# Performance work log

Measured on AMD Instinct MI355X. Metric: run time of the kernel, lower is better.

Reference implementation:

```python
import jax, jax.numpy as jnp
import numpy as np

K = 1024          # num_embeddings
D = 64            # embedding_dim
COMMIT = 0.25
DIVERSITY = 0.1


def setup_inputs() -> dict:
    key = jax.random.key(0)
    k1, k2 = jax.random.split(key)
    inputs = jax.random.normal(k1, (64, D, 32, 32), dtype=jnp.float32)
    emb = jax.random.uniform(k2, (K, D), dtype=jnp.float32,
                             minval=-1.0 / K, maxval=1.0 / K)
    return {"inputs": inputs, "emb": emb}


def reference(inputs, emb):
    # NCHW -> NHWC, flatten to [N, D]
    x = jnp.transpose(inputs, (0, 2, 3, 1))          # [B,H,W,D]
    flat = x.reshape(-1, D)                           # [N,D]

    dist = (jnp.sum(flat * flat, axis=1, keepdims=True)
            + jnp.sum(emb * emb, axis=1)
            - 2.0 * flat @ emb.T)
    idx = jnp.argmin(dist, axis=1)                    # [N]
    encodings = jax.nn.one_hot(idx, K, dtype=flat.dtype)  # [N,K]

    # codebook lookup (equivalent to encodings @ emb)
    quantized = jnp.take(emb, idx, axis=0).reshape(x.shape)  # [B,H,W,D]

    sg = jax.lax.stop_gradient
    e_latent_loss = jnp.mean((sg(quantized) - x) ** 2)
    q_latent_loss = jnp.mean((quantized - sg(x)) ** 2)

    avg_probs = jnp.mean(encodings, axis=0)           # [K]
    perplexity = jnp.exp(-jnp.sum(avg_probs * jnp.log(avg_probs + 1e-10)))
    diversity_loss = DIVERSITY * (K - perplexity) / K

    loss = q_latent_loss + COMMIT * e_latent_loss + diversity_loss

    # straight-through estimator
    quantized_st = x + sg(quantized - x)
    quant_out = jnp.transpose(quantized_st, (0, 3, 1, 2))  # NHWC -> NCHW

    return loss, quant_out, perplexity, encodings, idx[:, None]
```

## Files before the change

### kernel.cpp

```cpp
#include <hip/hip_runtime.h>
#include <math.h>

typedef _Float16 half8 __attribute__((ext_vector_type(8)));
typedef float floatx4 __attribute__((ext_vector_type(4)));

namespace {
constexpr int Kc = 1024;
constexpr int Dd = 64;
constexpr float MARGIN = 4e-4f;

__device__ inline float np_sumsq64_s(const float* __restrict__ a, int st) {
#pragma clang fp contract(off)
    float r[8];
    #pragma unroll
    for (int j = 0; j < 8; ++j) r[j] = a[j * st] * a[j * st];
    #pragma unroll
    for (int i = 8; i < 64; i += 8) {
        #pragma unroll
        for (int j = 0; j < 8; ++j) {
            float s = a[(i + j) * st] * a[(i + j) * st];
            r[j] = r[j] + s;
        }
    }
    return ((r[0] + r[1]) + (r[2] + r[3])) + ((r[4] + r[5]) + (r[6] + r[7]));
}

__device__ inline float np_dist(const float* __restrict__ x, int xs,
                                const float* __restrict__ emb, int k,
                                float xx, float eek) {
    const float* e = emb + (size_t)k * Dd;
    float g = 0.f;
    #pragma unroll
    for (int d = 0; d < Dd; ++d) g = fmaf(x[d * xs], e[d], g);
    float A = xx + eek;
    return fmaf(-2.f, g, A);
}

__global__ void k_prep(const float* __restrict__ emb, float* __restrict__ ee,
                       _Float16* __restrict__ emb16) {
    int k = blockIdx.x * blockDim.x + threadIdx.x;
    const float* e = emb + (size_t)k * Dd;
    ee[k] = np_sumsq64_s(e, 1);
    #pragma unroll
    for (int d = 0; d < Dd; ++d) emb16[k * Dd + d] = (_Float16)e[d];
}

__global__ __launch_bounds__(256, 4) void k_main(
    const float* __restrict__ inputs, const float* __restrict__ emb,
    const float* __restrict__ ee_g, const _Float16* __restrict__ emb16,
    float* __restrict__ quant, float* __restrict__ enc, float* __restrict__ idx_out,
    unsigned int* __restrict__ hist, float* __restrict__ partials)
{
    __shared__ float eeS[Kc];
    __shared__ float cD[64][16][2];
    __shared__ int   cI[64][16][2];
    __shared__ float red[64];
    __shared__ int   flagged[64];
    __shared__ int   nflag;
    __shared__ float fbD[256];
    __shared__ int   fbI[256];

    const int tid = threadIdx.x;
    const int w   = tid >> 6;
    const int ln  = tid & 63;
    const int lm  = ln & 15;
    const int lq  = ln >> 4;

    if (tid == 0) nflag = 0;
    #pragma unroll
    for (int i = 0; i < 4; ++i) eeS[tid + i * 256] = ee_g[tid + i * 256];

    const int nA = blockIdx.x * 64 + w * 16 + lm;
    const float* xA = inputs + (size_t)(nA >> 10) * (Dd * 1024) + (nA & 1023);
    half8 a0, a1;
    #pragma unroll
    for (int j = 0; j < 8; ++j) {
        a0[j] = (_Float16)xA[(lq * 8 + j) * 1024];
        a1[j] = (_Float16)xA[(lq * 8 + j + 32) * 1024];
    }

    __syncthreads();

    float4* enc4 = (float4*)enc + (size_t)blockIdx.x * 16384 + tid;

    float b1[4], b2[4];
    int   i1[4], i2[4];
    #pragma unroll
    for (int r = 0; r < 4; ++r) { b1[r] = INFINITY; b2[r] = INFINITY; i1[r] = 0; i2[r] = 0; }

    for (int t = 0; t < 64; ++t) {
        const int kn = t * 16 + lm;
        const half8 bb0 = *(const half8*)(emb16 + kn * Dd + lq * 8);
        const half8 bb1 = *(const half8*)(emb16 + kn * Dd + 32 + lq * 8);
        floatx4 acc = {0.f, 0.f, 0.f, 0.f};
        acc = __builtin_amdgcn_mfma_f32_16x16x32_f16(a0, bb0, acc, 0, 0, 0);
        acc = __builtin_amdgcn_mfma_f32_16x16x32_f16(a1, bb1, acc, 0, 0, 0);
        const float eev = eeS[kn];
        #pragma unroll
        for (int r = 0; r < 4; ++r) {
            float s = fmaf(-2.f, acc[r], eev);
            bool lt1 = s < b1[r], lt2 = s < b2[r];
            b2[r] = lt1 ? b1[r] : (lt2 ? s : b2[r]);
            i2[r] = lt1 ? i1[r] : (lt2 ? kn : i2[r]);
            b1[r] = lt1 ? s : b1[r];
            i1[r] = lt1 ? kn : i1[r];
        }
        *enc4 = float4{0.f, 0.f, 0.f, 0.f};
        enc4 += 256;
    }

    #pragma unroll
    for (int r = 0; r < 4; ++r) {
        int p = w * 16 + lq * 4 + r;
        cD[p][lm][0] = b1[r]; cI[p][lm][0] = i1[r];
        cD[p][lm][1] = b2[r]; cI[p][lm][1] = i2[r];
    }
    __syncthreads();

    if (tid < 64) {
        const int p = tid;
        const int n = blockIdx.x * 64 + p;
        const float* x = inputs + (size_t)(n >> 10) * (Dd * 1024) + (n & 1023);
        float amin = INFINITY;
        #pragma unroll
        for (int c = 0; c < 16; ++c) amin = fminf(amin, cD[p][c][0]);
        const float M = amin + MARGIN;
        bool flag = false;
        #pragma unroll
        for (int c = 0; c < 16; ++c) flag |= (cD[p][c][1] <= M);
        if (flag) {
            int s = atomicAdd(&nflag, 1);
            flagged[s] = p;
        } else {
            const float xx = np_sumsq64_s(x, 1024);
            float bd = INFINITY; int bi = 0x7fffffff;
            for (int c = 0; c < 16; ++c)
                #pragma unroll
                for (int s2 = 0; s2 < 2; ++s2)
                    if (cD[p][c][s2] <= M) {
                        int k = cI[p][c][s2];
                        float d = np_dist(x, 1024, emb, k, xx, eeS[k]);
                        if (d < bd || (d == bd && k < bi)) { bd = d; bi = k; }
                    }
            const float4* eb = (const float4*)(emb + (size_t)bi * Dd);
            float* qout = quant + (size_t)(n >> 10) * (Dd * 1024) + (n & 1023);
            #pragma unroll
            for (int i = 0; i < 16; ++i) {
                float4 v = eb[i];
                qout[(i * 4 + 0) * 1024] = v.x;
                qout[(i * 4 + 1) * 1024] = v.y;
                qout[(i * 4 + 2) * 1024] = v.z;
                qout[(i * 4 + 3) * 1024] = v.w;
            }
            idx_out[n] = (float)bi;
            atomicAdd(hist + bi, 1u);
            enc[(size_t)n * Kc + bi] = 1.0f;
            red[p] = bd;
        }
    }
    __syncthreads();

    const int nf = nflag;
    for (int f = 0; f < nf; ++f) {
        const int p = flagged[f];
        const int n = blockIdx.x * 64 + p;
        const float* x = inputs + (size_t)(n >> 10) * (Dd * 1024) + (n & 1023);
        const float xx = np_sumsq64_s(x, 1024);
        float bd = INFINITY; int bi = 0;
        #pragma unroll
        for (int q = 0; q < 4; ++q) {
            int k = tid * 4 + q;
            float d = np_dist(x, 1024, emb, k, xx, eeS[k]);
            bool lt = d < bd;
            bd = lt ? d : bd; bi = lt ? k : bi;
        }
        fbD[tid] = bd; fbI[tid] = bi;
        __syncthreads();
        if (tid == 0) {
            float gd = INFINITY; int gi = 0;
            for (int tt = 0; tt < 256; ++tt)
                if (fbD[tt] < gd) { gd = fbD[tt]; gi = fbI[tt]; }
            const float4* eb = (const float4*)(emb + (size_t)gi * Dd);
            float* qout = quant + (size_t)(n >> 10) * (Dd * 1024) + (n & 1023);
            for (int i = 0; i < 16; ++i) {
                float4 v = eb[i];
                qout[(i * 4 + 0) * 1024] = v.x;
                qout[(i * 4 + 1) * 1024] = v.y;
                qout[(i * 4 + 2) * 1024] = v.z;
                qout[(i * 4 + 3) * 1024] = v.w;
            }
            idx_out[n] = (float)gi;
            atomicAdd(hist + gi, 1u);
            enc[(size_t)n * Kc + gi] = 1.0f;
            red[p] = gd;
        }
        __syncthreads();
    }

    if (tid < 64) {
        float v = red[tid];
        #pragma unroll
        for (int off = 32; off > 0; off >>= 1) v += __shfl_down(v, off, 64);
        if (ln == 0) partials[blockIdx.x] = v;
    }
}

__global__ __launch_bounds__(1024) void k_fin(
    const unsigned int* __restrict__ hist, const float* __restrict__ partials,
    float* __restrict__ loss_out, float* __restrict__ perp_out)
{
    __shared__ double sd[1024];
    int tid = threadIdx.x;
    double p = (double)hist[tid] * (1.0 / 65536.0);
    sd[tid] = p * log(p + 1e-10);
    __syncthreads();
    for (int s = 512; s > 0; s >>= 1) {
        if (tid < s) sd[tid] += sd[tid + s];
        __syncthreads();
    }
    double ent = sd[0];
    __syncthreads();
    sd[tid] = (double)partials[tid];
    __syncthreads();
    for (int s = 512; s > 0; s >>= 1) {
        if (tid < s) sd[tid] += sd[tid + s];
        __syncthreads();
    }
    if (tid == 0) {
        double perp = exp(-ent);
        double mean = sd[0] * (1.0 / 4194304.0);
        double loss = 1.25 * mean + 0.1 * (1024.0 - perp) / 1024.0;
        loss_out[0] = (float)loss;
        perp_out[0] = (float)perp;
    }
}
}

extern "C" void kernel_launch(void* const* d_in, const int* in_sizes, int n_in,
                              void* d_out, int out_size, void* d_ws, size_t ws_size,
                              hipStream_t stream)
{
    const float* inputs = (const float*)d_in[0];
    const float* emb    = (const float*)d_in[1];
    float* out = (float*)d_out;

    float* loss_out = out;
    float* quant    = out + 1;
    float* perp_out = out + 1 + 4194304;
    float* enc      = out + 2 + 4194304;
    float* idx_out  = out + 2 + 4194304 + 67108864;

    unsigned int* hist = (unsigned int*)d_ws;
    float* partials    = (float*)d_ws + 1024;
    float* ee          = (float*)d_ws + 2048;
    _Float16* emb16    = (_Float16*)((float*)d_ws + 3072);

    hipMemsetAsync(d_ws, 0, 2048 * sizeof(float), stream);
    k_prep<<<Kc / 256, 256, 0, stream>>>(emb, ee, emb16);
    k_main<<<65536 / 64, 256, 0, stream>>>(inputs, emb, ee, emb16,
                                           quant, enc, idx_out, hist, partials);
    k_fin<<<1, 1024, 0, stream>>>(hist, partials, loss_out, perp_out);
}
```

Measured before the change: 491.7 us.

## Stage codebook tiles in LDS, transpose candidate arrays, parallelize quant writeout

The fp16 codebook is now loaded cooperatively into padded shared-memory tiles of 128 rows, and the MFMA B operands are read from there instead of directly from global memory. The per-pixel candidate arrays are transposed so the 64-thread scan reads them without LDS bank conflicts. The quantized-output write moves out of the single-thread and 64-thread paths into a final phase where all 256 threads write it. In exchange there are extra barriers per codebook chunk and more shared memory, which may lower occupancy.

```diff
diff --git a/kernel.cpp b/kernel.cpp
--- a/kernel.cpp
+++ b/kernel.cpp
@@ -51,14 +51,16 @@
     float* __restrict__ quant, float* __restrict__ enc, float* __restrict__ idx_out,
     unsigned int* __restrict__ hist, float* __restrict__ partials)
 {
-    __shared__ float eeS[Kc];
-    __shared__ float cD[64][16][2];
-    __shared__ int   cI[64][16][2];
-    __shared__ float red[64];
-    __shared__ int   flagged[64];
-    __shared__ int   nflag;
-    __shared__ float fbD[256];
-    __shared__ int   fbI[256];
+    __shared__ short  smemB[128 * 72];
+    __shared__ float  eeS[Kc];
+    __shared__ float  cDT[16][65], cD2T[16][65];
+    __shared__ int    cIT[16][65], cI2T[16][65];
+    __shared__ float  red[64];
+    __shared__ int    bidxS[64];
+    __shared__ int    flagged[64];
+    __shared__ int    nflag;
+    __shared__ float  fbD[256];
+    __shared__ int    fbI[256];
 
     const int tid = threadIdx.x;
     const int w   = tid >> 6;
@@ -79,8 +81,6 @@
         a1[j] = (_Float16)xA[(lq * 8 + j + 32) * 1024];
     }
 
-    __syncthreads();
-
     float4* enc4 = (float4*)enc + (size_t)blockIdx.x * 16384 + tid;
 
     float b1[4], b2[4];
@@ -88,32 +88,46 @@
     #pragma unroll
     for (int r = 0; r < 4; ++r) { b1[r] = INFINITY; b2[r] = INFINITY; i1[r] = 0; i2[r] = 0; }
 
-    for (int t = 0; t < 64; ++t) {
-        const int kn = t * 16 + lm;
-        const half8 bb0 = *(const half8*)(emb16 + kn * Dd + lq * 8);
-        const half8 bb1 = *(const half8*)(emb16 + kn * Dd + 32 + lq * 8);
-        floatx4 acc = {0.f, 0.f, 0.f, 0.f};
-        acc = __builtin_amdgcn_mfma_f32_16x16x32_f16(a0, bb0, acc, 0, 0, 0);
-        acc = __builtin_amdgcn_mfma_f32_16x16x32_f16(a1, bb1, acc, 0, 0, 0);
-        const float eev = eeS[kn];
-        #pragma unroll
-        for (int r = 0; r < 4; ++r) {
-            float s = fmaf(-2.f, acc[r], eev);
-            bool lt1 = s < b1[r], lt2 = s < b2[r];
-            b2[r] = lt1 ? b1[r] : (lt2 ? s : b2[r]);
-            i2[r] = lt1 ? i1[r] : (lt2 ? kn : i2[r]);
-            b1[r] = lt1 ? s : b1[r];
-            i1[r] = lt1 ? kn : i1[r];
-        }
-        *enc4 = float4{0.f, 0.f, 0.f, 0.f};
-        enc4 += 256;
+    for (int c = 0; c < 8; ++c) {
+        __syncthreads();
+        #pragma unroll
+        for (int u = 0; u < 4; ++u) {
+            int unit = u * 256 + tid;
+            int row = unit >> 3, c8 = unit & 7;
+            half8 v = *(const half8*)(emb16 + ((size_t)(c * 128 + row) * 64) + c8 * 8);
+            *(half8*)(smemB + row * 72 + c8 * 8) = v;
+        }
+        __syncthreads();
+
+        #pragma unroll
+        for (int tt = 0; tt < 8; ++tt) {
+            const int r = tt * 16 + lm;
+            const int kn = c * 128 + r;
+            const half8 bb0 = *(const half8*)(smemB + r * 72 + lq * 8);
+            const half8 bb1 = *(const half8*)(smemB + r * 72 + 32 + lq * 8);
+            floatx4 acc = {0.f, 0.f, 0.f, 0.f};
+            acc = __builtin_amdgcn_mfma_f32_16x16x32_f16(a0, bb0, acc, 0, 0, 0);
+            acc = __builtin_amdgcn_mfma_f32_16x16x32_f16(a1, bb1, acc, 0, 0, 0);
+            const float eev = eeS[kn];
+            #pragma unroll
+            for (int r4i = 0; r4i < 4; ++r4i) {
+                float s = fmaf(-2.f, acc[r4i], eev);
+                bool lt1 = s < b1[r4i], lt2 = s < b2[r4i];
+                b2[r4i] = lt1 ? b1[r4i] : (lt2 ? s : b2[r4i]);
+                i2[r4i] = lt1 ? i1[r4i] : (lt2 ? kn : i2[r4i]);
+                b1[r4i] = lt1 ? s : b1[r4i];
+                i1[r4i] = lt1 ? kn : i1[r4i];
+            }
+            *enc4 = float4{0.f, 0.f, 0.f, 0.f};
+            enc4 += 256;
+        }
     }
 
     #pragma unroll
     for (int r = 0; r < 4; ++r) {
         int p = w * 16 + lq * 4 + r;
-        cD[p][lm][0] = b1[r]; cI[p][lm][0] = i1[r];
-        cD[p][lm][1] = b2[r]; cI[p][lm][1] = i2[r];
+        cDT[lm][p] = b1[r]; cIT[lm][p] = i1[r];
+        cD2T[lm][p] = b2[r]; cI2T[lm][p] = i2[r];
     }
     __syncthreads();
 
@@ -123,39 +137,28 @@
         const float* x = inputs + (size_t)(n >> 10) * (Dd * 1024) + (n & 1023);
         float amin = INFINITY;
         #pragma unroll
-        for (int c = 0; c < 16; ++c) amin = fminf(amin, cD[p][c][0]);
+        for (int cc = 0; cc < 16; ++cc) amin = fminf(amin, cDT[cc][p]);
         const float M = amin + MARGIN;
         bool flag = false;
         #pragma unroll
-        for (int c = 0; c < 16; ++c) flag |= (cD[p][c][1] <= M);
+        for (int cc = 0; cc < 16; ++cc) flag |= (cD2T[cc][p] <= M);
         if (flag) {
             int s = atomicAdd(&nflag, 1);
             flagged[s] = p;
         } else {
             const float xx = np_sumsq64_s(x, 1024);
             float bd = INFINITY; int bi = 0x7fffffff;
-            for (int c = 0; c < 16; ++c)
-                #pragma unroll
-                for (int s2 = 0; s2 < 2; ++s2)
-                    if (cD[p][c][s2] <= M) {
-                        int k = cI[p][c][s2];
-                        float d = np_dist(x, 1024, emb, k, xx, eeS[k]);
-                        if (d < bd || (d == bd && k < bi)) { bd = d; bi = k; }
-                    }
-            const float4* eb = (const float4*)(emb + (size_t)bi * Dd);
-            float* qout = quant + (size_t)(n >> 10) * (Dd * 1024) + (n & 1023);
-            #pragma unroll
-            for (int i = 0; i < 16; ++i) {
-                float4 v = eb[i];
-                qout[(i * 4 + 0) * 1024] = v.x;
-                qout[(i * 4 + 1) * 1024] = v.y;
-                qout[(i * 4 + 2) * 1024] = v.z;
-                qout[(i * 4 + 3) * 1024] = v.w;
-            }
+            for (int cc = 0; cc < 16; ++cc)
+                if (cDT[cc][p] <= M) {
+                    int k = cIT[cc][p];
+                    float d = np_dist(x, 1024, emb, k, xx, eeS[k]);
+                    if (d < bd || (d == bd && k < bi)) { bd = d; bi = k; }
+                }
+            bidxS[p] = bi;
+            red[p] = bd;
             idx_out[n] = (float)bi;
             atomicAdd(hist + bi, 1u);
             enc[(size_t)n * Kc + bi] = 1.0f;
-            red[p] = bd;
         }
     }
     __syncthreads();
@@ -178,23 +181,31 @@
         __syncthreads();
         if (tid == 0) {
             float gd = INFINITY; int gi = 0;
-            for (int tt = 0; tt < 256; ++tt)
-                if (fbD[tt] < gd) { gd = fbD[tt]; gi = fbI[tt]; }
-            const float4* eb = (const float4*)(emb + (size_t)gi * Dd);
-            float* qout = quant + (size_t)(n >> 10) * (Dd * 1024) + (n & 1023);
-            for (int i = 0; i < 16; ++i) {
-                float4 v = eb[i];
-                qout[(i * 4 + 0) * 1024] = v.x;
-                qout[(i * 4 + 1) * 1024] = v.y;
-                qout[(i * 4 + 2) * 1024] = v.z;
-                qout[(i * 4 + 3) * 1024] = v.w;
-            }
+            for (int t2 = 0; t2 < 256; ++t2)
+                if (fbD[t2] < gd) { gd = fbD[t2]; gi = fbI[t2]; }
+            bidxS[p] = gi;
+            red[p] = gd;
             idx_out[n] = (float)gi;
             atomicAdd(hist + gi, 1u);
             enc[(size_t)n * Kc + gi] = 1.0f;
-            red[p] = gd;
-        }
-        __syncthreads();
+        }
+        __syncthreads();
+    }
+
+    {
+        const int n = blockIdx.x * 64 + ln;
+        const int bi = bidxS[ln];
+        float* qout = quant + (size_t)(n >> 10) * (Dd * 1024) + (n & 1023);
+        const float4* eb = (const float4*)(emb + (size_t)bi * Dd);
+        #pragma unroll
+        for (int i = 0; i < 4; ++i) {
+            float4 v = eb[w * 4 + i];
+            const int d0 = w * 16 + i * 4;
+            qout[(d0 + 0) * 1024] = v.x;
+            qout[(d0 + 1) * 1024] = v.y;
+            qout[(d0 + 2) * 1024] = v.z;
+            qout[(d0 + 3) * 1024] = v.w;
+        }
     }
 
     if (tid < 64) {
```

Result: faster. 459.2 us (-6.6%).
